# Kernel optimization log

Hardware: AMD Instinct MI355X
Metric: run time of the kernel (lower is better)

The kernel has to match this reference:

```python
import jax, jax.numpy as jnp
import numpy as np

EPS = 1e-10
NUM_RELATION = 4
N_NODES = 50000
N_EDGES = 800000
D_IN = 128
D_H = 256


def rgc_layer(x, src, dst, rel, rel_w, rel_b, loop_w, loop_b):
    # torchdrug RelationalGraphConv: scatter-mean per (node, relation), then
    # linear over concatenated per-relation features + self-loop linear + relu.
    N, d = x.shape
    msg = x[src]                                      # [E, d] gather
    idx = dst * NUM_RELATION + rel                    # [E] bucket per (node, relation)
    num_seg = N * NUM_RELATION
    agg = jax.ops.segment_sum(msg, idx, num_segments=num_seg)            # [N*R, d]
    cnt = jax.ops.segment_sum(jnp.ones((msg.shape[0], 1), x.dtype), idx,
                              num_segments=num_seg)                       # [N*R, 1]
    update = (agg / (cnt + EPS)).reshape(N, NUM_RELATION * d)            # [N, R*d]
    out = update @ rel_w + rel_b + x @ loop_w + loop_b                   # [N, d_out]
    return jax.nn.relu(out)


def highway(x, hp_w, hp_b, ht_w, ht_b):
    proj = jax.nn.relu(x @ hp_w + hp_b)
    gate = jax.nn.sigmoid(x @ ht_w + ht_b)
    return gate * proj + (1.0 - gate) * x


def setup_inputs() -> dict:
    key = jax.random.key(0)
    ks = jax.random.split(key, 16)
    s = 0.02
    inp = {
        "x": jax.random.normal(ks[0], (N_NODES, D_IN), dtype=jnp.float32),
        "src": jax.random.randint(ks[1], (N_EDGES,), 0, N_NODES, dtype=jnp.int32),
        "dst": jax.random.randint(ks[2], (N_EDGES,), 0, N_NODES, dtype=jnp.int32),
        "rel": jax.random.randint(ks[3], (N_EDGES,), 0, NUM_RELATION, dtype=jnp.int32),
        # layer 1: RGC(128->256) + Highway(256)
        "rel_w1": jax.random.normal(ks[4], (NUM_RELATION * D_IN, D_H), dtype=jnp.float32) * s,
        "rel_b1": jnp.zeros((D_H,), jnp.float32),
        "loop_w1": jax.random.normal(ks[5], (D_IN, D_H), dtype=jnp.float32) * s,
        "loop_b1": jnp.zeros((D_H,), jnp.float32),
        "hp_w1": jax.random.normal(ks[6], (D_H, D_H), dtype=jnp.float32) * s,
        "hp_b1": jnp.zeros((D_H,), jnp.float32),
        "ht_w1": jax.random.normal(ks[7], (D_H, D_H), dtype=jnp.float32) * s,
        "ht_b1": jnp.full((D_H,), -2.0, jnp.float32),  # transform.bias.data.fill_(-2.0)
        # layer 2: RGC(256->256) + Highway(256)
        "rel_w2": jax.random.normal(ks[8], (NUM_RELATION * D_H, D_H), dtype=jnp.float32) * s,
        "rel_b2": jnp.zeros((D_H,), jnp.float32),
        "loop_w2": jax.random.normal(ks[9], (D_H, D_H), dtype=jnp.float32) * s,
        "loop_b2": jnp.zeros((D_H,), jnp.float32),
        "hp_w2": jax.random.normal(ks[10], (D_H, D_H), dtype=jnp.float32) * s,
        "hp_b2": jnp.zeros((D_H,), jnp.float32),
        "ht_w2": jax.random.normal(ks[11], (D_H, D_H), dtype=jnp.float32) * s,
        "ht_b2": jnp.full((D_H,), -2.0, jnp.float32),
    }
    return inp


def reference(x, src, dst, rel,
              rel_w1, rel_b1, loop_w1, loop_b1, hp_w1, hp_b1, ht_w1, ht_b1,
              rel_w2, rel_b2, loop_w2, loop_b2, hp_w2, hp_b2, ht_w2, ht_b2):
    h = rgc_layer(x, src, dst, rel, rel_w1, rel_b1, loop_w1, loop_b1)
    h = highway(h, hp_w1, hp_b1, ht_w1, ht_b1)
    h = rgc_layer(h, src, dst, rel, rel_w2, rel_b2, loop_w2, loop_b2)
    h = highway(h, hp_w2, hp_b2, ht_w2, ht_b2)
    return h  # node_feature, shape [N, 256]
```

## Files before the change

### kernel.cpp

```cpp
#include <hip/hip_runtime.h>

typedef __bf16 bf16_t;
typedef __bf16 bf16x8 __attribute__((ext_vector_type(8)));
typedef __bf16 bf16x4 __attribute__((ext_vector_type(4)));
typedef float f32x4 __attribute__((ext_vector_type(4)));

#define BM 128
#define BN 128
#define BK 32

__device__ __forceinline__ void gload_lds16(const void* g, void* s) {
    __builtin_amdgcn_global_load_lds(
        (const __attribute__((address_space(1))) unsigned int*)g,
        (__attribute__((address_space(3))) unsigned int*)s, 16, 0, 0);
}

__global__ __launch_bounds__(256) void gemm_k(
    const bf16_t* __restrict__ A, int lda, int M,
    const bf16_t* __restrict__ Bt, int K,
    const float* __restrict__ bias, int relu_flag,
    bf16_t* __restrict__ outb, int ldo, int ocol)
{
    __shared__ __align__(16) bf16_t As[BM * BK];
    __shared__ __align__(16) bf16_t Bs[BN * BK];
    const int tid  = threadIdx.x;
    const int m0   = blockIdx.x * BM;
    const int n0   = blockIdx.y * BN;
    const int wave = tid >> 6, lane = tid & 63;
    const int wr   = wave >> 1, wc = wave & 1;
    const int lm   = lane & 15, quad = lane >> 4;

    f32x4 acc[4][4] = {};

    for (int k0 = 0; k0 < K; k0 += BK) {
        __syncthreads();
        #pragma unroll
        for (int j = 0; j < 2; j++) {
            int c   = wave * 128 + j * 64 + lane;
            int row = c >> 2;
            int col = (c & 3) << 3;
            int gm  = m0 + row; if (gm >= M) gm = M - 1;
            gload_lds16(A + (size_t)gm * lda + k0 + col,
                        As + (size_t)(wave * 128 + j * 64) * 8);
        }
        #pragma unroll
        for (int j = 0; j < 2; j++) {
            int c   = wave * 128 + j * 64 + lane;
            int row = c >> 2;
            int col = (c & 3) << 3;
            gload_lds16(Bt + (size_t)(n0 + row) * K + k0 + col,
                        Bs + (size_t)(wave * 128 + j * 64) * 8);
        }
        __syncthreads();

        bf16x8 af[4], bfr[4];
        #pragma unroll
        for (int i = 0; i < 4; i++)
            af[i] = *(const bf16x8*)&As[(wr * 64 + i * 16 + lm) * BK + quad * 8];
        #pragma unroll
        for (int i = 0; i < 4; i++)
            bfr[i] = *(const bf16x8*)&Bs[(wc * 64 + i * 16 + lm) * BK + quad * 8];
        #pragma unroll
        for (int mi = 0; mi < 4; mi++)
            #pragma unroll
            for (int ni = 0; ni < 4; ni++)
                acc[mi][ni] = __builtin_amdgcn_mfma_f32_16x16x32_bf16(
                    af[mi], bfr[ni], acc[mi][ni], 0, 0, 0);
    }

    #pragma unroll
    for (int mi = 0; mi < 4; mi++) {
        #pragma unroll
        for (int ni = 0; ni < 4; ni++) {
            int col = n0 + wc * 64 + ni * 16 + lm;
            float b = bias[col];
            #pragma unroll
            for (int r = 0; r < 4; r++) {
                int row = m0 + wr * 64 + mi * 16 + quad * 4 + r;
                if (row < M) {
                    float v = acc[mi][ni][r] + b;
                    if (relu_flag) v = fmaxf(v, 0.f);
                    outb[(size_t)row * ldo + ocol + col] = (bf16_t)v;
                }
            }
        }
    }
}

__global__ void count_k(const int* __restrict__ dst, const int* __restrict__ rel,
                        int* __restrict__ cnt, int E)
{
    int e = blockIdx.x * blockDim.x + threadIdx.x;
    if (e < E) atomicAdd(&cnt[dst[e] * 4 + rel[e]], 1);
}

__global__ void scan_partial(const int* __restrict__ cnt, int* __restrict__ offs,
                             int* __restrict__ chunkSums, int NSEG)
{
    __shared__ int sh[256];
    int t = threadIdx.x;
    int idx = blockIdx.x * 256 + t;
    int v = (idx < NSEG) ? cnt[idx] : 0;
    sh[t] = v;
    __syncthreads();
    for (int d = 1; d < 256; d <<= 1) {
        int add = (t >= d) ? sh[t - d] : 0;
        __syncthreads();
        sh[t] += add;
        __syncthreads();
    }
    if (idx < NSEG) offs[idx] = sh[t] - v;
    if (t == 255) chunkSums[blockIdx.x] = sh[t];
}

__global__ void scan_chunks(int* __restrict__ chunkSums, int NCHUNK)
{
    __shared__ int sh[1024];
    int t = threadIdx.x;
    int v = (t < NCHUNK) ? chunkSums[t] : 0;
    sh[t] = v;
    __syncthreads();
    for (int d = 1; d < 1024; d <<= 1) {
        int add = (t >= d) ? sh[t - d] : 0;
        __syncthreads();
        sh[t] += add;
        __syncthreads();
    }
    if (t < NCHUNK) chunkSums[t] = sh[t] - v;
}

__global__ void scan_add(int* __restrict__ offs, const int* __restrict__ chunkSums,
                         int* __restrict__ cursor, int NSEG)
{
    int idx = blockIdx.x * 256 + threadIdx.x;
    if (idx < NSEG) {
        int o = offs[idx] + chunkSums[blockIdx.x];
        offs[idx] = o;
        cursor[idx] = o;
    }
}

__global__ void fill_k(const int* __restrict__ src, const int* __restrict__ dst,
                       const int* __restrict__ rel,
                       int* __restrict__ cursor, int* __restrict__ eidx, int E)
{
    int e = blockIdx.x * blockDim.x + threadIdx.x;
    if (e < E) {
        int seg = dst[e] * 4 + rel[e];
        int pos = atomicAdd(&cursor[seg], 1);
        eidx[pos] = src[e];
    }
}

__global__ void seg_mean256(const int* __restrict__ offs, const int* __restrict__ cnt,
                            const int* __restrict__ eidx,
                            const bf16_t* __restrict__ xb, int ldx,
                            bf16_t* __restrict__ Aout, int lda, int NSEG)
{
    int wv = (blockIdx.x << 2) + (threadIdx.x >> 6);
    if (wv >= NSEG) return;
    int lane = threadIdx.x & 63;
    int c = lane << 2;
    int start = offs[wv];
    int n = cnt[wv];
    f32x4 acc = {};
    int i = 0;
    for (; i + 4 <= n; i += 4) {
        int s0 = eidx[start + i + 0];
        int s1 = eidx[start + i + 1];
        int s2 = eidx[start + i + 2];
        int s3 = eidx[start + i + 3];
        bf16x4 v0 = *(const bf16x4*)(xb + (size_t)s0 * ldx + c);
        bf16x4 v1 = *(const bf16x4*)(xb + (size_t)s1 * ldx + c);
        bf16x4 v2 = *(const bf16x4*)(xb + (size_t)s2 * ldx + c);
        bf16x4 v3 = *(const bf16x4*)(xb + (size_t)s3 * ldx + c);
        #pragma unroll
        for (int j = 0; j < 4; j++)
            acc[j] += ((float)v0[j] + (float)v1[j]) + ((float)v2[j] + (float)v3[j]);
    }
    for (; i < n; i++) {
        int s = eidx[start + i];
        bf16x4 v = *(const bf16x4*)(xb + (size_t)s * ldx + c);
        #pragma unroll
        for (int j = 0; j < 4; j++) acc[j] += (float)v[j];
    }
    float inv = 1.0f / ((float)n + 1e-10f);
    int node = wv >> 2, r = wv & 3;
    bf16x4 o;
    o[0] = (bf16_t)(acc[0] * inv);
    o[1] = (bf16_t)(acc[1] * inv);
    o[2] = (bf16_t)(acc[2] * inv);
    o[3] = (bf16_t)(acc[3] * inv);
    *(bf16x4*)(Aout + (size_t)node * lda + r * 256 + c) = o;
}

__global__ void seg_mean128(const int* __restrict__ offs, const int* __restrict__ cnt,
                            const int* __restrict__ eidx,
                            const bf16_t* __restrict__ xb, int ldx,
                            bf16_t* __restrict__ Aout, int lda, int NSEG)
{
    int wv = (blockIdx.x << 2) + (threadIdx.x >> 6);
    if (wv >= NSEG) return;
    int lane = threadIdx.x & 63;
    int half = lane >> 5;
    int c = (lane & 31) << 2;
    int start = offs[wv];
    int n = cnt[wv];
    f32x4 acc = {};
    int i = 0;
    for (; i + 4 <= n; i += 4) {
        int s0 = eidx[start + i + half];
        int s1 = eidx[start + i + 2 + half];
        bf16x4 v0 = *(const bf16x4*)(xb + (size_t)s0 * ldx + c);
        bf16x4 v1 = *(const bf16x4*)(xb + (size_t)s1 * ldx + c);
        #pragma unroll
        for (int j = 0; j < 4; j++) acc[j] += (float)v0[j] + (float)v1[j];
    }
    for (; i + 2 <= n; i += 2) {
        int s = eidx[start + i + half];
        bf16x4 v = *(const bf16x4*)(xb + (size_t)s * ldx + c);
        #pragma unroll
        for (int j = 0; j < 4; j++) acc[j] += (float)v[j];
    }
    if (i < n && half == 0) {
        int s = eidx[start + i];
        bf16x4 v = *(const bf16x4*)(xb + (size_t)s * ldx + c);
        #pragma unroll
        for (int j = 0; j < 4; j++) acc[j] += (float)v[j];
    }
    #pragma unroll
    for (int j = 0; j < 4; j++) acc[j] += __shfl_xor(acc[j], 32, 64);
    if (half == 0) {
        float inv = 1.0f / ((float)n + 1e-10f);
        int node = wv >> 2, r = wv & 3;
        bf16x4 o;
        o[0] = (bf16_t)(acc[0] * inv);
        o[1] = (bf16_t)(acc[1] * inv);
        o[2] = (bf16_t)(acc[2] * inv);
        o[3] = (bf16_t)(acc[3] * inv);
        *(bf16x4*)(Aout + (size_t)node * lda + r * 128 + c) = o;
    }
}

__global__ void convert_x_k(const float* __restrict__ x, bf16_t* __restrict__ A1, int N)
{
    int t = blockIdx.x * blockDim.x + threadIdx.x;
    if (t >= N * 32) return;
    int row = t >> 5;
    int c = (t & 31) << 2;
    f32x4 v = *(const f32x4*)(x + (size_t)row * 128 + c);
    bf16x4 o;
    o[0] = (bf16_t)v[0]; o[1] = (bf16_t)v[1]; o[2] = (bf16_t)v[2]; o[3] = (bf16_t)v[3];
    *(bf16x4*)(A1 + (size_t)row * 640 + 512 + c) = o;
}

__global__ void transpose_w(const float* __restrict__ W, bf16_t* __restrict__ Wt,
                            int K, int ldk, int k0, int n0)
{
    int t = blockIdx.x * blockDim.x + threadIdx.x;
    if (t >= K * 256) return;
    int k = t >> 8, n = t & 255;
    Wt[(size_t)(n0 + n) * ldk + k0 + k] = (bf16_t)W[(size_t)k * 256 + n];
}

__global__ void prep_bias(const float* rb1, const float* lb1,
                          const float* rb2, const float* lb2,
                          const float* hpb1, const float* htb1,
                          const float* hpb2, const float* htb2,
                          float* bR1, float* bR2, float* bH1, float* bH2)
{
    int t = threadIdx.x;
    bR1[t] = rb1[t] + lb1[t];
    bR2[t] = rb2[t] + lb2[t];
    bH1[t] = hpb1[t]; bH1[256 + t] = htb1[t];
    bH2[t] = hpb2[t]; bH2[256 + t] = htb2[t];
}

__global__ void highway_k(const bf16_t* __restrict__ PG, const bf16_t* __restrict__ h,
                          int N, bf16_t* __restrict__ outb, int ldo, int ocol,
                          float* __restrict__ outf)
{
    int t = blockIdx.x * blockDim.x + threadIdx.x;
    if (t >= N * 64) return;
    int row = t >> 6;
    int c = (t & 63) << 2;
    size_t ip = (size_t)row * 512 + c;
    bf16x4 p = *(const bf16x4*)(PG + ip);
    bf16x4 g = *(const bf16x4*)(PG + ip + 256);
    bf16x4 hv = *(const bf16x4*)(h + (size_t)row * 256 + c);
    bf16x4 ob;
    f32x4 of;
    #pragma unroll
    for (int j = 0; j < 4; j++) {
        float gg = 1.0f / (1.0f + __expf(-(float)g[j]));
        float pp = fmaxf((float)p[j], 0.f);
        float v = gg * pp + (1.0f - gg) * (float)hv[j];
        ob[j] = (bf16_t)v;
        of[j] = v;
    }
    if (outb) *(bf16x4*)(outb + (size_t)row * ldo + ocol + c) = ob;
    if (outf) *(f32x4*)(outf + (size_t)row * 256 + c) = of;
}

extern "C" void kernel_launch(void* const* d_in, const int* in_sizes, int n_in,
                              void* d_out, int out_size, void* d_ws, size_t ws_size,
                              hipStream_t stream)
{
    const float* x       = (const float*)d_in[0];
    const int*   src     = (const int*)d_in[1];
    const int*   dst     = (const int*)d_in[2];
    const int*   rel     = (const int*)d_in[3];
    const float* rel_w1  = (const float*)d_in[4];
    const float* rel_b1  = (const float*)d_in[5];
    const float* loop_w1 = (const float*)d_in[6];
    const float* loop_b1 = (const float*)d_in[7];
    const float* hp_w1   = (const float*)d_in[8];
    const float* hp_b1   = (const float*)d_in[9];
    const float* ht_w1   = (const float*)d_in[10];
    const float* ht_b1   = (const float*)d_in[11];
    const float* rel_w2  = (const float*)d_in[12];
    const float* rel_b2  = (const float*)d_in[13];
    const float* loop_w2 = (const float*)d_in[14];
    const float* loop_b2 = (const float*)d_in[15];
    const float* hp_w2   = (const float*)d_in[16];
    const float* hp_b2   = (const float*)d_in[17];
    const float* ht_w2   = (const float*)d_in[18];
    const float* ht_b2   = (const float*)d_in[19];

    const int N = in_sizes[0] / 128;
    const int E = in_sizes[1];
    const int NSEG = N * 4;
    const int NCHUNK = (NSEG + 255) / 256;
    float* out = (float*)d_out;

    char* ws = (char*)d_ws;
    size_t off = 0;
    auto alloc = [&](size_t bytes) {
        void* p = ws + off;
        off += (bytes + 255) & ~(size_t)255;
        return p;
    };
    int*    cnt    = (int*)alloc((size_t)NSEG * 4);
    int*    offs   = (int*)alloc((size_t)NSEG * 4);
    int*    cursor = (int*)alloc((size_t)NSEG * 4);
    int*    chunkS = (int*)alloc(4096);
    int*    eidx   = (int*)alloc((size_t)E * 4);
    bf16_t* A1     = (bf16_t*)alloc((size_t)N * 640 * 2);
    bf16_t* A2     = (bf16_t*)alloc((size_t)N * 1280 * 2);
    bf16_t* h      = (bf16_t*)alloc((size_t)N * 256 * 2);
    bf16_t* W1t    = (bf16_t*)alloc((size_t)256 * 640 * 2);
    bf16_t* W2t    = (bf16_t*)alloc((size_t)256 * 1280 * 2);
    bf16_t* Wh1t   = (bf16_t*)alloc((size_t)512 * 256 * 2);
    bf16_t* Wh2t   = (bf16_t*)alloc((size_t)512 * 256 * 2);
    float*  bR1    = (float*)alloc(256 * 4);
    float*  bR2    = (float*)alloc(256 * 4);
    float*  bH1    = (float*)alloc(512 * 4);
    float*  bH2    = (float*)alloc(512 * 4);
    bf16_t* PG     = A1;

    dim3 blk(256);
    const int mtiles = (N + BM - 1) / BM;

    transpose_w<<<dim3(512), blk, 0, stream>>>(rel_w1, W1t, 512, 640, 0, 0);
    transpose_w<<<dim3(128), blk, 0, stream>>>(loop_w1, W1t, 128, 640, 512, 0);
    transpose_w<<<dim3(1024), blk, 0, stream>>>(rel_w2, W2t, 1024, 1280, 0, 0);
    transpose_w<<<dim3(256), blk, 0, stream>>>(loop_w2, W2t, 256, 1280, 1024, 0);
    transpose_w<<<dim3(256), blk, 0, stream>>>(hp_w1, Wh1t, 256, 256, 0, 0);
    transpose_w<<<dim3(256), blk, 0, stream>>>(ht_w1, Wh1t, 256, 256, 0, 256);
    transpose_w<<<dim3(256), blk, 0, stream>>>(hp_w2, Wh2t, 256, 256, 0, 0);
    transpose_w<<<dim3(256), blk, 0, stream>>>(ht_w2, Wh2t, 256, 256, 0, 256);
    prep_bias<<<dim3(1), blk, 0, stream>>>(rel_b1, loop_b1, rel_b2, loop_b2,
                                           hp_b1, ht_b1, hp_b2, ht_b2,
                                           bR1, bR2, bH1, bH2);
    convert_x_k<<<dim3((N * 32 + 255) / 256), blk, 0, stream>>>(x, A1, N);

    hipMemsetAsync(cnt, 0, (size_t)NSEG * 4, stream);
    count_k<<<dim3((E + 255) / 256), blk, 0, stream>>>(dst, rel, cnt, E);
    scan_partial<<<dim3(NCHUNK), blk, 0, stream>>>(cnt, offs, chunkS, NSEG);
    scan_chunks<<<dim3(1), dim3(1024), 0, stream>>>(chunkS, NCHUNK);
    scan_add<<<dim3(NCHUNK), blk, 0, stream>>>(offs, chunkS, cursor, NSEG);
    fill_k<<<dim3((E + 255) / 256), blk, 0, stream>>>(src, dst, rel, cursor, eidx, E);

    seg_mean128<<<dim3((NSEG + 3) / 4), blk, 0, stream>>>(offs, cnt, eidx,
                                                          A1 + 512, 640, A1, 640, NSEG);
    gemm_k<<<dim3(mtiles, 2), blk, 0, stream>>>(A1, 640, N, W1t, 640,
                                                bR1, 1, h, 256, 0);
    gemm_k<<<dim3(mtiles, 4), blk, 0, stream>>>(h, 256, N, Wh1t, 256,
                                                bH1, 0, PG, 512, 0);
    highway_k<<<dim3((N * 64 + 255) / 256), blk, 0, stream>>>(PG, h, N,
                                                              A2, 1280, 1024, nullptr);

    seg_mean256<<<dim3((NSEG + 3) / 4), blk, 0, stream>>>(offs, cnt, eidx,
                                                          A2 + 1024, 1280, A2, 1280, NSEG);
    gemm_k<<<dim3(mtiles, 2), blk, 0, stream>>>(A2, 1280, N, W2t, 1280,
                                                bR2, 1, h, 256, 0);
    gemm_k<<<dim3(mtiles, 4), blk, 0, stream>>>(h, 256, N, Wh2t, 256,
                                                bH2, 0, PG, 512, 0);
    highway_k<<<dim3((N * 64 + 255) / 256), blk, 0, stream>>>(PG, h, N,
                                                              nullptr, 0, 0, out);
}
```

Before: 616.5 us.

## Double GEMM K-tile, swizzle LDS layout, and remap blocks across XCDs

The GEMM kernel now uses a K tile of 64 instead of 32, halving the number of barrier-separated loop iterations. It stores A and B in shared memory with an XOR swizzle to avoid bank conflicts on the wider rows. Global addresses are precomputed once per block rather than every iteration. The launch is now a 1D grid that assigns adjacent M tiles to the same XCD and keeps all N tiles of a row block together, aiming for better L2 reuse of A. This doubles shared memory per block and adds padded blocks that exit early.

```diff
diff --git a/kernel.cpp b/kernel.cpp
--- a/kernel.cpp
+++ b/kernel.cpp
@@ -7,7 +7,7 @@
 
 #define BM 128
 #define BN 128
-#define BK 32
+#define BK 64
 
 __device__ __forceinline__ void gload_lds16(const void* g, void* s) {
     __builtin_amdgcn_global_load_lds(
@@ -19,53 +19,72 @@
     const bf16_t* __restrict__ A, int lda, int M,
     const bf16_t* __restrict__ Bt, int K,
     const float* __restrict__ bias, int relu_flag,
-    bf16_t* __restrict__ outb, int ldo, int ocol)
+    bf16_t* __restrict__ outb, int ldo, int ocol,
+    int NTM, int NTN)
 {
     __shared__ __align__(16) bf16_t As[BM * BK];
     __shared__ __align__(16) bf16_t Bs[BN * BK];
+
+    const int L    = blockIdx.x;
+    const int xcd  = L & 7;
+    const int rest = L >> 3;
+    const int nt   = rest % NTN;
+    const int sup  = rest / NTN;
+    const int mt   = sup * 8 + xcd;
+    if (mt >= NTM) return;
+    const int m0 = mt * BM;
+    const int n0 = nt * BN;
+
     const int tid  = threadIdx.x;
-    const int m0   = blockIdx.x * BM;
-    const int n0   = blockIdx.y * BN;
     const int wave = tid >> 6, lane = tid & 63;
     const int wr   = wave >> 1, wc = wave & 1;
     const int lm   = lane & 15, quad = lane >> 4;
 
+    const bf16_t* ag[4];
+    const bf16_t* bg[4];
+    #pragma unroll
+    for (int j = 0; j < 4; j++) {
+        int c    = wave * 256 + j * 64 + lane;
+        int row  = c >> 3;
+        int cc   = (c & 7) ^ (row & 7);
+        int col  = cc << 3;
+        int gm   = m0 + row; if (gm >= M) gm = M - 1;
+        ag[j] = A  + (size_t)gm * lda + col;
+        bg[j] = Bt + (size_t)(n0 + row) * K + col;
+    }
+
     f32x4 acc[4][4] = {};
 
     for (int k0 = 0; k0 < K; k0 += BK) {
         __syncthreads();
         #pragma unroll
-        for (int j = 0; j < 2; j++) {
-            int c   = wave * 128 + j * 64 + lane;
-            int row = c >> 2;
-            int col = (c & 3) << 3;
-            int gm  = m0 + row; if (gm >= M) gm = M - 1;
-            gload_lds16(A + (size_t)gm * lda + k0 + col,
-                        As + (size_t)(wave * 128 + j * 64) * 8);
+        for (int j = 0; j < 4; j++)
+            gload_lds16(ag[j] + k0, As + (size_t)(wave * 256 + j * 64) * 8);
+        #pragma unroll
+        for (int j = 0; j < 4; j++)
+            gload_lds16(bg[j] + k0, Bs + (size_t)(wave * 256 + j * 64) * 8);
+        __syncthreads();
+
+        #pragma unroll
+        for (int h = 0; h < 2; h++) {
+            bf16x8 af[4], bfr[4];
+            #pragma unroll
+            for (int i = 0; i < 4; i++) {
+                int r = wr * 64 + i * 16 + lm;
+                af[i] = *(const bf16x8*)&As[(size_t)(r * 8 + ((h * 4 + quad) ^ (r & 7))) * 8];
+            }
+            #pragma unroll
+            for (int i = 0; i < 4; i++) {
+                int r = wc * 64 + i * 16 + lm;
+                bfr[i] = *(const bf16x8*)&Bs[(size_t)(r * 8 + ((h * 4 + quad) ^ (r & 7))) * 8];
+            }
+            #pragma unroll
+            for (int mi = 0; mi < 4; mi++)
+                #pragma unroll
+                for (int ni = 0; ni < 4; ni++)
+                    acc[mi][ni] = __builtin_amdgcn_mfma_f32_16x16x32_bf16(
+                        af[mi], bfr[ni], acc[mi][ni], 0, 0, 0);
         }
-        #pragma unroll
-        for (int j = 0; j < 2; j++) {
-            int c   = wave * 128 + j * 64 + lane;
-            int row = c >> 2;
-            int col = (c & 3) << 3;
-            gload_lds16(Bt + (size_t)(n0 + row) * K + k0 + col,
-                        Bs + (size_t)(wave * 128 + j * 64) * 8);
-        }
-        __syncthreads();
-
-        bf16x8 af[4], bfr[4];
-        #pragma unroll
-        for (int i = 0; i < 4; i++)
-            af[i] = *(const bf16x8*)&As[(wr * 64 + i * 16 + lm) * BK + quad * 8];
-        #pragma unroll
-        for (int i = 0; i < 4; i++)
-            bfr[i] = *(const bf16x8*)&Bs[(wc * 64 + i * 16 + lm) * BK + quad * 8];
-        #pragma unroll
-        for (int mi = 0; mi < 4; mi++)
-            #pragma unroll
-            for (int ni = 0; ni < 4; ni++)
-                acc[mi][ni] = __builtin_amdgcn_mfma_f32_16x16x32_bf16(
-                    af[mi], bfr[ni], acc[mi][ni], 0, 0, 0);
     }
 
     #pragma unroll
@@ -359,7 +378,10 @@
     bf16_t* PG     = A1;
 
     dim3 blk(256);
-    const int mtiles = (N + BM - 1) / BM;
+    const int NTM = (N + BM - 1) / BM;
+    const int supers = (NTM + 7) / 8;
+    const int gridRGC = supers * 8 * 2;
+    const int gridHW  = supers * 8 * 4;
 
     transpose_w<<<dim3(512), blk, 0, stream>>>(rel_w1, W1t, 512, 640, 0, 0);
     transpose_w<<<dim3(128), blk, 0, stream>>>(loop_w1, W1t, 128, 640, 512, 0);
@@ -383,19 +405,19 @@
 
     seg_mean128<<<dim3((NSEG + 3) / 4), blk, 0, stream>>>(offs, cnt, eidx,
                                                           A1 + 512, 640, A1, 640, NSEG);
-    gemm_k<<<dim3(mtiles, 2), blk, 0, stream>>>(A1, 640, N, W1t, 640,
-                                                bR1, 1, h, 256, 0);
-    gemm_k<<<dim3(mtiles, 4), blk, 0, stream>>>(h, 256, N, Wh1t, 256,
-                                                bH1, 0, PG, 512, 0);
+    gemm_k<<<dim3(gridRGC), blk, 0, stream>>>(A1, 640, N, W1t, 640,
+                                              bR1, 1, h, 256, 0, NTM, 2);
+    gemm_k<<<dim3(gridHW), blk, 0, stream>>>(h, 256, N, Wh1t, 256,
+                                             bH1, 0, PG, 512, 0, NTM, 4);
     highway_k<<<dim3((N * 64 + 255) / 256), blk, 0, stream>>>(PG, h, N,
                                                               A2, 1280, 1024, nullptr);
 
     seg_mean256<<<dim3((NSEG + 3) / 4), blk, 0, stream>>>(offs, cnt, eidx,
                                                           A2 + 1024, 1280, A2, 1280, NSEG);
-    gemm_k<<<dim3(mtiles, 2), blk, 0, stream>>>(A2, 1280, N, W2t, 1280,
-                                                bR2, 1, h, 256, 0);
-    gemm_k<<<dim3(mtiles, 4), blk, 0, stream>>>(h, 256, N, Wh2t, 256,
-                                                bH2, 0, PG, 512, 0);
+    gemm_k<<<dim3(gridRGC), blk, 0, stream>>>(A2, 1280, N, W2t, 1280,
+                                              bR2, 1, h, 256, 0, NTM, 2);
+    gemm_k<<<dim3(gridHW), blk, 0, stream>>>(h, 256, N, Wh2t, 256,
+                                             bH2, 0, PG, 512, 0, NTM, 4);
     highway_k<<<dim3((N * 64 + 255) / 256), blk, 0, stream>>>(PG, h, N,
                                                               nullptr, 0, 0, out);
 }
```

Result: faster. 582.1 us (-5.6%).
